# Optimization experiments

Hardware: AMD Instinct MI355X
Metric: run time of the kernel (lower is better)

The kernel has to match this reference:

```python
import jax, jax.numpy as jnp
import numpy as np

N = 100000
E = 1600000
D_IN = 128
D_H = 256


def setup_inputs() -> dict:
    key = jax.random.key(0)
    ks = jax.random.split(key, 8)
    x = jax.random.normal(ks[0], (N, D_IN), dtype=jnp.float32)
    x_tilde = jax.random.normal(ks[1], (N, D_IN), dtype=jnp.float32)
    adj_row = jnp.sort(jax.random.randint(ks[2], (E,), 0, N, dtype=jnp.int32))
    adj_col = jax.random.randint(ks[3], (E,), 0, N, dtype=jnp.int32)
    # normalized-ish positive edge weights
    adj_vals = jax.random.uniform(ks[4], (E,), dtype=jnp.float32) / 16.0
    # Linear weight (torch layout [out, in]), xavier-ish scale
    W1 = jax.random.normal(ks[5], (D_H, D_IN), dtype=jnp.float32) * (2.0 / (D_IN + D_H)) ** 0.5
    prelu_a = jnp.full((1,), 0.25, dtype=jnp.float32)  # PReLU default slope
    w_bil = jax.random.normal(ks[6], (D_H, D_H), dtype=jnp.float32) * (2.0 / (2 * D_H)) ** 0.5
    return {"x": x, "x_tilde": x_tilde, "adj_vals": adj_vals, "adj_row": adj_row,
            "adj_col": adj_col, "W1": W1, "prelu_a": prelu_a, "w_bil": w_bil}


def reference(x, x_tilde, adj_vals, adj_row, adj_col, W1, prelu_a, w_bil):
    n = x.shape[0]

    def gcn(feat):
        # SpMM: agg[r] = sum_e vals[e] * feat[col[e]] for edges with row[e]==r
        gathered = adj_vals[:, None] * feat[adj_col]  # [E, D_IN]
        agg = jax.ops.segment_sum(gathered, adj_row, num_segments=n)  # [N, D_IN]
        z = agg @ W1.T  # [N, D_H]
        return jnp.where(z >= 0, z, prelu_a[0] * z)  # PReLU

    h = gcn(x)
    h_tilde = gcn(x_tilde)
    s = jax.nn.sigmoid(jnp.mean(h, axis=0))  # [D_H] readout (same for every row)
    dp = jnp.einsum('ni,ij,j->n', h, w_bil, s)  # bilinear discriminator
    dn = jnp.einsum('ni,ij,j->n', h_tilde, w_bil, s)
    return jnp.concatenate([dp, dn])[None, :]  # [1, 2N]
```

## Files before the change

kernel.cpp:

```cpp
#include <hip/hip_runtime.h>

__device__ __forceinline__ float b2f(unsigned short s) {
    union { unsigned int u; float f; } c; c.u = ((unsigned int)s) << 16; return c.f;
}
__device__ __forceinline__ unsigned short f2b(float f) {
    union { float f; unsigned int u; } c; c.f = f;
    unsigned int u = c.u;
    unsigned int r = u + 0x7FFFu + ((u >> 16) & 1u);
    return (unsigned short)(r >> 16);
}
__device__ __forceinline__ unsigned int pack2(float lo, float hi) {
    return ((unsigned int)f2b(hi) << 16) | f2b(lo);
}

typedef __attribute__((ext_vector_type(8))) short bf16x8;
typedef __attribute__((ext_vector_type(4))) float f32x4;

#define T_TILES 10

__global__ void detect_dtype(const unsigned int* __restrict__ xw,
                             int* __restrict__ flag, float* __restrict__ sum_h) {
    __shared__ int c;
    int tid = threadIdx.x;
    if (tid == 0) c = 0;
    sum_h[tid] = 0.f;
    __syncthreads();
    int cnt = 0;
    for (int i = tid; i < 1024; i += 256) {
        unsigned int w = xw[i];
        unsigned int e = (w >> 7) & 0xFFu;
        if (e >= 0x90u) cnt++;
    }
    atomicAdd(&c, cnt);
    __syncthreads();
    if (tid == 0) flag[0] = (c > 100) ? 1 : 0;
}

__global__ void build_rowptr(const int* __restrict__ row, int* __restrict__ rp,
                             int n, int e) {
    int i = blockIdx.x * blockDim.x + threadIdx.x;
    if (i > e) return;
    if (i == 0) {
        int r1 = row[0];
        for (int rr = 0; rr <= r1; ++rr) rp[rr] = 0;
    } else if (i == e) {
        int r0 = row[e - 1];
        for (int rr = r0 + 1; rr <= n; ++rr) rp[rr] = e;
    } else {
        int r0 = row[i - 1], r1 = row[i];
        for (int rr = r0 + 1; rr <= r1; ++rr) rp[rr] = i;
    }
}

__global__ void conv_params(const void* __restrict__ w1, const void* __restrict__ wbil,
                            const void* __restrict__ pa, const int* __restrict__ flag,
                            unsigned short* __restrict__ w1b, float* __restrict__ wbilf,
                            float* __restrict__ paf) {
    int i = blockIdx.x * blockDim.x + threadIdx.x;
    if (flag[0]) {
        if (i < 32768) w1b[i] = f2b(((const float*)w1)[i]);
        wbilf[i] = ((const float*)wbil)[i];
        if (i == 0) paf[0] = ((const float*)pa)[0];
    } else {
        if (i < 32768) w1b[i] = ((const unsigned short*)w1)[i];
        wbilf[i] = b2f(((const unsigned short*)wbil)[i]);
        if (i == 0) paf[0] = b2f(((const unsigned short*)pa)[0]);
    }
}

__global__ __launch_bounds__(256) void conv_x(
    const void* __restrict__ src0, const void* __restrict__ src1,
    const int* __restrict__ flag,
    unsigned short* __restrict__ d0, unsigned short* __restrict__ d1, int total8)
{
    const void* s = blockIdx.y ? src1 : src0;
    unsigned short* d = blockIdx.y ? d1 : d0;
    int i = blockIdx.x * 256 + threadIdx.x;
    if (i >= total8) return;
    if (flag[0]) {
        const float4* p = (const float4*)s + (size_t)i * 2;
        float4 a = p[0], b = p[1];
        uint4 o;
        o.x = pack2(a.x, a.y); o.y = pack2(a.z, a.w);
        o.z = pack2(b.x, b.y); o.w = pack2(b.z, b.w);
        ((uint4*)d)[i] = o;
    } else {
        ((uint4*)d)[i] = ((const uint4*)s)[i];
    }
}

__global__ __launch_bounds__(256) void spmm_dual2(
    const unsigned short* __restrict__ xb, const unsigned short* __restrict__ xtb,
    const void* __restrict__ valsv, const int* __restrict__ col,
    const int* __restrict__ row_ptr, const int* __restrict__ flag,
    unsigned short* __restrict__ aggx, unsigned short* __restrict__ aggt, int n)
{
    int wave = threadIdx.x >> 6;
    int lane = threadIdx.x & 63;
    int g = lane >> 4, l = lane & 15;
    int r = blockIdx.x * 4 + wave;
    if (r >= n) return;
    int e0 = row_ptr[r], e1 = row_ptr[r + 1];
    int f = flag[0];
    const float* valsf = (const float*)valsv;
    const unsigned short* valsb = (const unsigned short*)valsv;
    float ax[8], at[8];
#pragma unroll
    for (int d = 0; d < 8; ++d) { ax[d] = 0.f; at[d] = 0.f; }
    for (int base = e0; base < e1; base += 4) {
        int e = base + g;
        bool valid = (e < e1);
        int ec = valid ? e : (e1 - 1);
        int c = col[ec];
        float v = valid ? (f ? valsf[ec] : b2f(valsb[ec])) : 0.f;
        uint4 wx = ((const uint4*)(xb + (size_t)c * 128))[l];
        uint4 wt = ((const uint4*)(xtb + (size_t)c * 128))[l];
        ax[0] = fmaf(v, b2f((unsigned short)wx.x), ax[0]);
        ax[1] = fmaf(v, b2f((unsigned short)(wx.x >> 16)), ax[1]);
        ax[2] = fmaf(v, b2f((unsigned short)wx.y), ax[2]);
        ax[3] = fmaf(v, b2f((unsigned short)(wx.y >> 16)), ax[3]);
        ax[4] = fmaf(v, b2f((unsigned short)wx.z), ax[4]);
        ax[5] = fmaf(v, b2f((unsigned short)(wx.z >> 16)), ax[5]);
        ax[6] = fmaf(v, b2f((unsigned short)wx.w), ax[6]);
        ax[7] = fmaf(v, b2f((unsigned short)(wx.w >> 16)), ax[7]);
        at[0] = fmaf(v, b2f((unsigned short)wt.x), at[0]);
        at[1] = fmaf(v, b2f((unsigned short)(wt.x >> 16)), at[1]);
        at[2] = fmaf(v, b2f((unsigned short)wt.y), at[2]);
        at[3] = fmaf(v, b2f((unsigned short)(wt.y >> 16)), at[3]);
        at[4] = fmaf(v, b2f((unsigned short)wt.z), at[4]);
        at[5] = fmaf(v, b2f((unsigned short)(wt.z >> 16)), at[5]);
        at[6] = fmaf(v, b2f((unsigned short)wt.w), at[6]);
        at[7] = fmaf(v, b2f((unsigned short)(wt.w >> 16)), at[7]);
    }
#pragma unroll
    for (int d = 0; d < 8; ++d) {
        ax[d] += __shfl_xor(ax[d], 16, 64);
        ax[d] += __shfl_xor(ax[d], 32, 64);
        at[d] += __shfl_xor(at[d], 16, 64);
        at[d] += __shfl_xor(at[d], 32, 64);
    }
    if (g == 0) {
        uint4 o;
        o.x = pack2(ax[0], ax[1]); o.y = pack2(ax[2], ax[3]);
        o.z = pack2(ax[4], ax[5]); o.w = pack2(ax[6], ax[7]);
        ((uint4*)(aggx + (size_t)r * 128))[l] = o;
    } else if (g == 1) {
        uint4 o;
        o.x = pack2(at[0], at[1]); o.y = pack2(at[2], at[3]);
        o.z = pack2(at[4], at[5]); o.w = pack2(at[6], at[7]);
        ((uint4*)(aggt + (size_t)r * 128))[l] = o;
    }
}

__global__ __launch_bounds__(256) void spmm_dual_legacy(
    const void* __restrict__ xv, const void* __restrict__ xtv,
    const void* __restrict__ valsv, const int* __restrict__ col,
    const int* __restrict__ row_ptr, const int* __restrict__ flag,
    unsigned short* __restrict__ aggx, unsigned short* __restrict__ aggt, int n)
{
    int wave = threadIdx.x >> 6;
    int lane = threadIdx.x & 63;
    int r = blockIdx.x * 4 + wave;
    if (r >= n) return;
    int e0 = row_ptr[r], e1 = row_ptr[r + 1];
    float ax0 = 0.f, ax1 = 0.f, at0 = 0.f, at1 = 0.f;
    if (flag[0]) {
        const float* x  = (const float*)xv;
        const float* xt = (const float*)xtv;
        const float* vals = (const float*)valsv;
        for (int e = e0; e < e1; ++e) {
            int c = col[e];
            float v = vals[e];
            float2 wx = ((const float2*)(x + (size_t)c * 128))[lane];
            float2 wt = ((const float2*)(xt + (size_t)c * 128))[lane];
            ax0 = fmaf(v, wx.x, ax0); ax1 = fmaf(v, wx.y, ax1);
            at0 = fmaf(v, wt.x, at0); at1 = fmaf(v, wt.y, at1);
        }
    } else {
        const unsigned short* x  = (const unsigned short*)xv;
        const unsigned short* xt = (const unsigned short*)xtv;
        const unsigned short* vals = (const unsigned short*)valsv;
        for (int e = e0; e < e1; ++e) {
            int c = col[e];
            float v = b2f(vals[e]);
            unsigned int wx = ((const unsigned int*)(x + (size_t)c * 128))[lane];
            unsigned int wt = ((const unsigned int*)(xt + (size_t)c * 128))[lane];
            ax0 = fmaf(v, b2f((unsigned short)wx), ax0);
            ax1 = fmaf(v, b2f((unsigned short)(wx >> 16)), ax1);
            at0 = fmaf(v, b2f((unsigned short)wt), at0);
            at1 = fmaf(v, b2f((unsigned short)(wt >> 16)), at1);
        }
    }
    ((unsigned int*)(aggx + (size_t)r * 128))[lane] = pack2(ax0, ax1);
    ((unsigned int*)(aggt + (size_t)r * 128))[lane] = pack2(at0, at1);
}

__global__ __launch_bounds__(256) void gemm_colsum2(
    const short* __restrict__ aggb, const short* __restrict__ w1,
    const float* __restrict__ paf, float* __restrict__ sum_h, int ntiles)
{
    int tid = threadIdx.x;
    int w = tid >> 6, lane = tid & 63;
    int nl = lane & 15, quad = lane >> 4;
    const short* brow = w1 + ((size_t)(4 * w) * 16 + nl) * 128 + quad * 8;
    bf16x8 bf[4][4];
#pragma unroll
    for (int j = 0; j < 4; ++j)
#pragma unroll
        for (int k = 0; k < 4; ++k)
            bf[j][k] = *(const bf16x8*)(brow + j * 2048 + k * 32);
    float aslope = paf[0];
    float cs[4] = {0.f, 0.f, 0.f, 0.f};
    int t0 = blockIdx.x * T_TILES;
    int nt = ntiles - t0; if (nt > T_TILES) nt = T_TILES;
    for (int i = 0; i < nt; ++i) {
        const short* arow = aggb + ((size_t)(t0 + i) * 16 + nl) * 128 + quad * 8;
        bf16x8 af[4];
#pragma unroll
        for (int k = 0; k < 4; ++k) af[k] = *(const bf16x8*)(arow + k * 32);
        f32x4 acc[4];
#pragma unroll
        for (int j = 0; j < 4; ++j) acc[j] = (f32x4){0.f, 0.f, 0.f, 0.f};
#pragma unroll
        for (int k = 0; k < 4; ++k)
#pragma unroll
            for (int j = 0; j < 4; ++j)
                acc[j] = __builtin_amdgcn_mfma_f32_16x16x32_bf16(af[k], bf[j][k], acc[j], 0, 0, 0);
#pragma unroll
        for (int j = 0; j < 4; ++j)
#pragma unroll
            for (int r = 0; r < 4; ++r) {
                float z = acc[j][r];
                cs[j] += (z >= 0.f) ? z : aslope * z;
            }
    }
#pragma unroll
    for (int j = 0; j < 4; ++j) {
        cs[j] += __shfl_xor(cs[j], 16, 64);
        cs[j] += __shfl_xor(cs[j], 32, 64);
    }
    if (quad == 0)
#pragma unroll
        for (int j = 0; j < 4; ++j)
            atomicAdd(&sum_h[(4 * w + j) * 16 + nl], cs[j]);
}

__global__ __launch_bounds__(256) void compute_v(
    const float* __restrict__ sum_h, const float* __restrict__ wbilf,
    float* __restrict__ v, float invN)
{
    __shared__ float s_lds[256];
    int t = threadIdx.x;
    float m = sum_h[t] * invN;
    s_lds[t] = 1.f / (1.f + expf(-m));
    __syncthreads();
    const float* wrow = wbilf + (size_t)t * 256;
    float acc = 0.f;
#pragma unroll 8
    for (int j = 0; j < 256; ++j)
        acc = fmaf(wrow[j], s_lds[j], acc);
    v[t] = acc;
}

__global__ __launch_bounds__(256) void gemm_dp2(
    const short* __restrict__ aggx, const short* __restrict__ aggt,
    const short* __restrict__ w1, const float* __restrict__ paf,
    const float* __restrict__ v, const int* __restrict__ flag,
    void* __restrict__ outv, int ntiles, int N)
{
    __shared__ float dpbuf[4][T_TILES * 16];
    int tid = threadIdx.x;
    int w = tid >> 6, lane = tid & 63;
    int nl = lane & 15, quad = lane >> 4;
    const short* agg = blockIdx.y ? aggt : aggx;
    const short* brow = w1 + ((size_t)(4 * w) * 16 + nl) * 128 + quad * 8;
    bf16x8 bf[4][4];
#pragma unroll
    for (int j = 0; j < 4; ++j)
#pragma unroll
        for (int k = 0; k < 4; ++k)
            bf[j][k] = *(const bf16x8*)(brow + j * 2048 + k * 32);
    float vreg[4];
#pragma unroll
    for (int j = 0; j < 4; ++j) vreg[j] = v[(4 * w + j) * 16 + nl];
    float aslope = paf[0];
    int t0 = blockIdx.x * T_TILES;
    int nt = ntiles - t0; if (nt > T_TILES) nt = T_TILES;
    for (int i = 0; i < nt; ++i) {
        const short* arow = agg + ((size_t)(t0 + i) * 16 + nl) * 128 + quad * 8;
        bf16x8 af[4];
#pragma unroll
        for (int k = 0; k < 4; ++k) af[k] = *(const bf16x8*)(arow + k * 32);
        f32x4 acc[4];
#pragma unroll
        for (int j = 0; j < 4; ++j) acc[j] = (f32x4){0.f, 0.f, 0.f, 0.f};
#pragma unroll
        for (int k = 0; k < 4; ++k)
#pragma unroll
            for (int j = 0; j < 4; ++j)
                acc[j] = __builtin_amdgcn_mfma_f32_16x16x32_bf16(af[k], bf[j][k], acc[j], 0, 0, 0);
        float p[4] = {0.f, 0.f, 0.f, 0.f};
#pragma unroll
        for (int j = 0; j < 4; ++j)
#pragma unroll
            for (int r = 0; r < 4; ++r) {
                float z = acc[j][r];
                float h = (z >= 0.f) ? z : aslope * z;
                p[r] = fmaf(h, vreg[j], p[r]);
            }
#pragma unroll
        for (int r = 0; r < 4; ++r) {
            p[r] += __shfl_xor(p[r], 1, 64);
            p[r] += __shfl_xor(p[r], 2, 64);
            p[r] += __shfl_xor(p[r], 4, 64);
            p[r] += __shfl_xor(p[r], 8, 64);
        }
        if (nl == 0)
#pragma unroll
            for (int r = 0; r < 4; ++r)
                dpbuf[w][i * 16 + quad * 4 + r] = p[r];
    }
    __syncthreads();
    int nloc = nt * 16;
    int f = flag[0];
    for (int idx = tid; idx < nloc; idx += 256) {
        float s = dpbuf[0][idx] + dpbuf[1][idx] + dpbuf[2][idx] + dpbuf[3][idx];
        size_t o = (size_t)blockIdx.y * N + (size_t)t0 * 16 + idx;
        if (f) ((float*)outv)[o] = s;
        else   ((unsigned short*)outv)[o] = f2b(s);
    }
}

extern "C" void kernel_launch(void* const* d_in, const int* in_sizes, int n_in,
                              void* d_out, int out_size, void* d_ws, size_t ws_size,
                              hipStream_t stream) {
    const void* x    = d_in[0];
    const void* xt   = d_in[1];
    const void* vals = d_in[2];
    const int* row   = (const int*)d_in[3];
    const int* col   = (const int*)d_in[4];
    const void* w1   = d_in[5];
    const void* pa   = d_in[6];
    const void* wb   = d_in[7];

    const int N = in_sizes[0] / 128;
    const int E = in_sizes[2];
    const int ntiles = (N + 15) / 16;

    char* ws = (char*)d_ws;
    size_t off = 0;
    auto alloc = [&](size_t bytes) { char* p = ws + off; off = (off + bytes + 255) & ~(size_t)255; return p; };
    int* row_ptr         = (int*)alloc((size_t)(N + 1) * 4);
    unsigned short* aggx = (unsigned short*)alloc((size_t)N * 128 * 2);
    unsigned short* aggt = (unsigned short*)alloc((size_t)N * 128 * 2);
    unsigned short* w1b  = (unsigned short*)alloc(32768 * 2);
    float* wbilf         = (float*)alloc(65536 * 4);
    float* sum_h         = (float*)alloc(256 * 4);
    float* vvec          = (float*)alloc(256 * 4);
    float* paf           = (float*)alloc(4);
    int* flag            = (int*)alloc(4);
    size_t xbBytes = (size_t)N * 128 * 2;
    bool big = (off + 2 * xbBytes + 512) <= ws_size;
    unsigned short* xb  = nullptr;
    unsigned short* xtb = nullptr;
    if (big) {
        xb  = (unsigned short*)alloc(xbBytes);
        xtb = (unsigned short*)alloc(xbBytes);
    }

    detect_dtype<<<1, 256, 0, stream>>>((const unsigned int*)x, flag, sum_h);
    build_rowptr<<<(E + 1 + 255) / 256, 256, 0, stream>>>(row, row_ptr, N, E);
    conv_params<<<256, 256, 0, stream>>>(w1, wb, pa, flag, w1b, wbilf, paf);
    if (big) {
        int total8 = (N * 128) / 8;
        conv_x<<<dim3((total8 + 255) / 256, 2), 256, 0, stream>>>(x, xt, flag, xb, xtb, total8);
        spmm_dual2<<<(N + 3) / 4, 256, 0, stream>>>(xb, xtb, vals, col, row_ptr, flag, aggx, aggt, N);
    } else {
        spmm_dual_legacy<<<(N + 3) / 4, 256, 0, stream>>>(x, xt, vals, col, row_ptr, flag, aggx, aggt, N);
    }
    gemm_colsum2<<<(ntiles + T_TILES - 1) / T_TILES, 256, 0, stream>>>(
        (const short*)aggx, (const short*)w1b, paf, sum_h, ntiles);
    compute_v<<<1, 256, 0, stream>>>(sum_h, wbilf, vvec, 1.0f / (float)N);
    gemm_dp2<<<dim3((ntiles + T_TILES - 1) / T_TILES, 2), 256, 0, stream>>>(
        (const short*)aggx, (const short*)aggt, (const short*)w1b, paf, vvec, flag,
        d_out, ntiles, N);
}
```

Before: 349.4 us.

## Interleave x/x_tilde rows, fuse prep kernels, unroll SpMM, replace atomics with partials

Converts x and x_tilde into one interleaved bf16 buffer, so each gathered column index hits a contiguous 512-byte row holding both feature sets. The row-pointer build, parameter conversion and input conversion are merged into one prep kernel to cut launches. The SpMM loop now processes two edges per group per iteration with the dtype branch hoisted out of the loop. The column-sum kernel writes per-block partials that compute_v reduces, replacing atomics and the sum_h zeroing, and T_TILES doubles to 20. Risks are a longer serial partial reduction in the single-block compute_v2, fewer blocks in the GEMM kernels, and higher register pressure in the SpMM.

```diff
diff --git a/kernel.cpp b/kernel.cpp
--- a/kernel.cpp
+++ b/kernel.cpp
@@ -12,18 +12,26 @@
 __device__ __forceinline__ unsigned int pack2(float lo, float hi) {
     return ((unsigned int)f2b(hi) << 16) | f2b(lo);
 }
+__device__ __forceinline__ void fma8(float* a, float v, uint4 w) {
+    a[0] = fmaf(v, b2f((unsigned short)w.x), a[0]);
+    a[1] = fmaf(v, b2f((unsigned short)(w.x >> 16)), a[1]);
+    a[2] = fmaf(v, b2f((unsigned short)w.y), a[2]);
+    a[3] = fmaf(v, b2f((unsigned short)(w.y >> 16)), a[3]);
+    a[4] = fmaf(v, b2f((unsigned short)w.z), a[4]);
+    a[5] = fmaf(v, b2f((unsigned short)(w.z >> 16)), a[5]);
+    a[6] = fmaf(v, b2f((unsigned short)w.w), a[6]);
+    a[7] = fmaf(v, b2f((unsigned short)(w.w >> 16)), a[7]);
+}
 
 typedef __attribute__((ext_vector_type(8))) short bf16x8;
 typedef __attribute__((ext_vector_type(4))) float f32x4;
 
-#define T_TILES 10
-
-__global__ void detect_dtype(const unsigned int* __restrict__ xw,
-                             int* __restrict__ flag, float* __restrict__ sum_h) {
+#define T_TILES 20
+
+__global__ void detect_dtype(const unsigned int* __restrict__ xw, int* __restrict__ flag) {
     __shared__ int c;
     int tid = threadIdx.x;
     if (tid == 0) c = 0;
-    sum_h[tid] = 0.f;
     __syncthreads();
     int cnt = 0;
     for (int i = tid; i < 1024; i += 256) {
@@ -36,63 +44,64 @@
     if (tid == 0) flag[0] = (c > 100) ? 1 : 0;
 }
 
-__global__ void build_rowptr(const int* __restrict__ row, int* __restrict__ rp,
-                             int n, int e) {
-    int i = blockIdx.x * blockDim.x + threadIdx.x;
-    if (i > e) return;
-    if (i == 0) {
-        int r1 = row[0];
-        for (int rr = 0; rr <= r1; ++rr) rp[rr] = 0;
-    } else if (i == e) {
-        int r0 = row[e - 1];
-        for (int rr = r0 + 1; rr <= n; ++rr) rp[rr] = e;
+__global__ __launch_bounds__(256) void prep(
+    const int* __restrict__ row, int* __restrict__ rp, int n, int e, int rb,
+    const void* __restrict__ w1, const void* __restrict__ wbil,
+    const void* __restrict__ pa, const int* __restrict__ flag,
+    unsigned short* __restrict__ w1b, float* __restrict__ wbilf, float* __restrict__ paf,
+    int pb,
+    const void* __restrict__ x, const void* __restrict__ xt,
+    unsigned short* __restrict__ xint, int total8, int halfcb)
+{
+    int b = blockIdx.x, tid = threadIdx.x;
+    if (b < rb) {
+        int i = b * 256 + tid;
+        if (i > e) return;
+        if (i == 0) {
+            int r1 = row[0];
+            for (int rr = 0; rr <= r1; ++rr) rp[rr] = 0;
+        } else if (i == e) {
+            int r0 = row[e - 1];
+            for (int rr = r0 + 1; rr <= n; ++rr) rp[rr] = e;
+        } else {
+            int r0 = row[i - 1], r1 = row[i];
+            for (int rr = r0 + 1; rr <= r1; ++rr) rp[rr] = i;
+        }
+    } else if (b < rb + pb) {
+        int i = (b - rb) * 256 + tid;
+        if (flag[0]) {
+            if (i < 32768) w1b[i] = f2b(((const float*)w1)[i]);
+            wbilf[i] = ((const float*)wbil)[i];
+            if (i == 0) paf[0] = ((const float*)pa)[0];
+        } else {
+            if (i < 32768) w1b[i] = ((const unsigned short*)w1)[i];
+            wbilf[i] = b2f(((const unsigned short*)wbil)[i]);
+            if (i == 0) paf[0] = b2f(((const unsigned short*)pa)[0]);
+        }
     } else {
-        int r0 = row[i - 1], r1 = row[i];
-        for (int rr = r0 + 1; rr <= r1; ++rr) rp[rr] = i;
-    }
-}
-
-__global__ void conv_params(const void* __restrict__ w1, const void* __restrict__ wbil,
-                            const void* __restrict__ pa, const int* __restrict__ flag,
-                            unsigned short* __restrict__ w1b, float* __restrict__ wbilf,
-                            float* __restrict__ paf) {
-    int i = blockIdx.x * blockDim.x + threadIdx.x;
-    if (flag[0]) {
-        if (i < 32768) w1b[i] = f2b(((const float*)w1)[i]);
-        wbilf[i] = ((const float*)wbil)[i];
-        if (i == 0) paf[0] = ((const float*)pa)[0];
-    } else {
-        if (i < 32768) w1b[i] = ((const unsigned short*)w1)[i];
-        wbilf[i] = b2f(((const unsigned short*)wbil)[i]);
-        if (i == 0) paf[0] = b2f(((const unsigned short*)pa)[0]);
-    }
-}
-
-__global__ __launch_bounds__(256) void conv_x(
-    const void* __restrict__ src0, const void* __restrict__ src1,
+        int cb = b - rb - pb;
+        int which = (cb >= halfcb) ? 1 : 0;
+        int i = (cb - which * halfcb) * 256 + tid;
+        if (i >= total8) return;
+        const void* s = which ? xt : x;
+        int node = i >> 4, sub = i & 15;
+        uint4 o;
+        if (flag[0]) {
+            const float4* p = (const float4*)s + (size_t)i * 2;
+            float4 a = p[0], bb = p[1];
+            o.x = pack2(a.x, a.y);  o.y = pack2(a.z, a.w);
+            o.z = pack2(bb.x, bb.y); o.w = pack2(bb.z, bb.w);
+        } else {
+            o = ((const uint4*)s)[i];
+        }
+        *(uint4*)(xint + (size_t)node * 256 + which * 128 + sub * 8) = o;
+    }
+}
+
+__global__ __launch_bounds__(256) void spmm_dual3(
+    const unsigned short* __restrict__ xint, const void* __restrict__ valsv,
+    const int* __restrict__ col, const int* __restrict__ row_ptr,
     const int* __restrict__ flag,
-    unsigned short* __restrict__ d0, unsigned short* __restrict__ d1, int total8)
-{
-    const void* s = blockIdx.y ? src1 : src0;
-    unsigned short* d = blockIdx.y ? d1 : d0;
-    int i = blockIdx.x * 256 + threadIdx.x;
-    if (i >= total8) return;
-    if (flag[0]) {
-        const float4* p = (const float4*)s + (size_t)i * 2;
-        float4 a = p[0], b = p[1];
-        uint4 o;
-        o.x = pack2(a.x, a.y); o.y = pack2(a.z, a.w);
-        o.z = pack2(b.x, b.y); o.w = pack2(b.z, b.w);
-        ((uint4*)d)[i] = o;
-    } else {
-        ((uint4*)d)[i] = ((const uint4*)s)[i];
-    }
-}
-
-__global__ __launch_bounds__(256) void spmm_dual2(
-    const unsigned short* __restrict__ xb, const unsigned short* __restrict__ xtb,
-    const void* __restrict__ valsv, const int* __restrict__ col,
-    const int* __restrict__ row_ptr, const int* __restrict__ flag,
     unsigned short* __restrict__ aggx, unsigned short* __restrict__ aggt, int n)
 {
     int wave = threadIdx.x >> 6;
@@ -101,36 +110,41 @@
     int r = blockIdx.x * 4 + wave;
     if (r >= n) return;
     int e0 = row_ptr[r], e1 = row_ptr[r + 1];
-    int f = flag[0];
-    const float* valsf = (const float*)valsv;
-    const unsigned short* valsb = (const unsigned short*)valsv;
     float ax[8], at[8];
 #pragma unroll
     for (int d = 0; d < 8; ++d) { ax[d] = 0.f; at[d] = 0.f; }
-    for (int base = e0; base < e1; base += 4) {
-        int e = base + g;
-        bool valid = (e < e1);
-        int ec = valid ? e : (e1 - 1);
-        int c = col[ec];
-        float v = valid ? (f ? valsf[ec] : b2f(valsb[ec])) : 0.f;
-        uint4 wx = ((const uint4*)(xb + (size_t)c * 128))[l];
-        uint4 wt = ((const uint4*)(xtb + (size_t)c * 128))[l];
-        ax[0] = fmaf(v, b2f((unsigned short)wx.x), ax[0]);
-        ax[1] = fmaf(v, b2f((unsigned short)(wx.x >> 16)), ax[1]);
-        ax[2] = fmaf(v, b2f((unsigned short)wx.y), ax[2]);
-        ax[3] = fmaf(v, b2f((unsigned short)(wx.y >> 16)), ax[3]);
-        ax[4] = fmaf(v, b2f((unsigned short)wx.z), ax[4]);
-        ax[5] = fmaf(v, b2f((unsigned short)(wx.z >> 16)), ax[5]);
-        ax[6] = fmaf(v, b2f((unsigned short)wx.w), ax[6]);
-        ax[7] = fmaf(v, b2f((unsigned short)(wx.w >> 16)), ax[7]);
-        at[0] = fmaf(v, b2f((unsigned short)wt.x), at[0]);
-        at[1] = fmaf(v, b2f((unsigned short)(wt.x >> 16)), at[1]);
-        at[2] = fmaf(v, b2f((unsigned short)wt.y), at[2]);
-        at[3] = fmaf(v, b2f((unsigned short)(wt.y >> 16)), at[3]);
-        at[4] = fmaf(v, b2f((unsigned short)wt.z), at[4]);
-        at[5] = fmaf(v, b2f((unsigned short)(wt.z >> 16)), at[5]);
-        at[6] = fmaf(v, b2f((unsigned short)wt.w), at[6]);
-        at[7] = fmaf(v, b2f((unsigned short)(wt.w >> 16)), at[7]);
+    if (flag[0]) {
+        const float* vals = (const float*)valsv;
+        for (int base = e0; base < e1; base += 8) {
+            int eA = base + g, eB = base + 4 + g;
+            bool vA = eA < e1, vB = eB < e1;
+            int ecA = vA ? eA : e1 - 1, ecB = vB ? eB : e1 - 1;
+            int cA = col[ecA], cB = col[ecB];
+            float fvA = vA ? vals[ecA] : 0.f;
+            float fvB = vB ? vals[ecB] : 0.f;
+            const uint4* pA = (const uint4*)(xint + (size_t)cA * 256);
+            const uint4* pB = (const uint4*)(xint + (size_t)cB * 256);
+            uint4 xA = pA[l], tA = pA[16 + l];
+            uint4 xB = pB[l], tB = pB[16 + l];
+            fma8(ax, fvA, xA); fma8(at, fvA, tA);
+            fma8(ax, fvB, xB); fma8(at, fvB, tB);
+        }
+    } else {
+        const unsigned short* vals = (const unsigned short*)valsv;
+        for (int base = e0; base < e1; base += 8) {
+            int eA = base + g, eB = base + 4 + g;
+            bool vA = eA < e1, vB = eB < e1;
+            int ecA = vA ? eA : e1 - 1, ecB = vB ? eB : e1 - 1;
+            int cA = col[ecA], cB = col[ecB];
+            float fvA = vA ? b2f(vals[ecA]) : 0.f;
+            float fvB = vB ? b2f(vals[ecB]) : 0.f;
+            const uint4* pA = (const uint4*)(xint + (size_t)cA * 256);
+            const uint4* pB = (const uint4*)(xint + (size_t)cB * 256);
+            uint4 xA = pA[l], tA = pA[16 + l];
+            uint4 xB = pB[l], tB = pB[16 + l];
+            fma8(ax, fvA, xA); fma8(at, fvA, tA);
+            fma8(ax, fvB, xB); fma8(at, fvB, tB);
+        }
     }
 #pragma unroll
     for (int d = 0; d < 8; ++d) {
@@ -195,9 +209,9 @@
     ((unsigned int*)(aggt + (size_t)r * 128))[lane] = pack2(at0, at1);
 }
 
-__global__ __launch_bounds__(256) void gemm_colsum2(
+__global__ __launch_bounds__(256) void gemm_colsum3(
     const short* __restrict__ aggb, const short* __restrict__ w1,
-    const float* __restrict__ paf, float* __restrict__ sum_h, int ntiles)
+    const float* __restrict__ paf, float* __restrict__ partial, int ntiles)
 {
     int tid = threadIdx.x;
     int w = tid >> 6, lane = tid & 63;
@@ -242,17 +256,19 @@
     if (quad == 0)
 #pragma unroll
         for (int j = 0; j < 4; ++j)
-            atomicAdd(&sum_h[(4 * w + j) * 16 + nl], cs[j]);
-}
-
-__global__ __launch_bounds__(256) void compute_v(
-    const float* __restrict__ sum_h, const float* __restrict__ wbilf,
-    float* __restrict__ v, float invN)
+            partial[(size_t)blockIdx.x * 256 + (4 * w + j) * 16 + nl] = cs[j];
+}
+
+__global__ __launch_bounds__(256) void compute_v2(
+    const float* __restrict__ partial, int nblocks,
+    const float* __restrict__ wbilf, float* __restrict__ v, float invN)
 {
     __shared__ float s_lds[256];
     int t = threadIdx.x;
-    float m = sum_h[t] * invN;
-    s_lds[t] = 1.f / (1.f + expf(-m));
+    float s = 0.f;
+    for (int b = 0; b < nblocks; ++b)
+        s += partial[(size_t)b * 256 + t];
+    s_lds[t] = 1.f / (1.f + expf(-s * invN));
     __syncthreads();
     const float* wrow = wbilf + (size_t)t * 256;
     float acc = 0.f;
@@ -346,6 +362,7 @@
     const int N = in_sizes[0] / 128;
     const int E = in_sizes[2];
     const int ntiles = (N + 15) / 16;
+    const int cs_blocks = (ntiles + T_TILES - 1) / T_TILES;
 
     char* ws = (char*)d_ws;
     size_t off = 0;
@@ -355,33 +372,37 @@
     unsigned short* aggt = (unsigned short*)alloc((size_t)N * 128 * 2);
     unsigned short* w1b  = (unsigned short*)alloc(32768 * 2);
     float* wbilf         = (float*)alloc(65536 * 4);
-    float* sum_h         = (float*)alloc(256 * 4);
+    float* partial       = (float*)alloc((size_t)cs_blocks * 256 * 4);
     float* vvec          = (float*)alloc(256 * 4);
     float* paf           = (float*)alloc(4);
     int* flag            = (int*)alloc(4);
-    size_t xbBytes = (size_t)N * 128 * 2;
-    bool big = (off + 2 * xbBytes + 512) <= ws_size;
-    unsigned short* xb  = nullptr;
-    unsigned short* xtb = nullptr;
+    size_t xintBytes = (size_t)N * 256 * 2;
+    bool big = (off + xintBytes + 512) <= ws_size;
+    unsigned short* xint = nullptr;
+    if (big) xint = (unsigned short*)alloc(xintBytes);
+
+    detect_dtype<<<1, 256, 0, stream>>>((const unsigned int*)x, flag);
+
+    int rb = (E + 1 + 255) / 256;
+    int pb = 256;
+    int total8 = (N * 128) / 8;
+    int halfcb = big ? (total8 + 255) / 256 : 0;
+    prep<<<rb + pb + 2 * halfcb, 256, 0, stream>>>(
+        row, row_ptr, N, E, rb,
+        w1, wb, pa, flag, w1b, wbilf, paf, pb,
+        x, xt, xint, total8, halfcb);
+
     if (big) {
-        xb  = (unsigned short*)alloc(xbBytes);
-        xtb = (unsigned short*)alloc(xbBytes);
-    }
-
-    detect_dtype<<<1, 256, 0, stream>>>((const unsigned int*)x, flag, sum_h);
-    build_rowptr<<<(E + 1 + 255) / 256, 256, 0, stream>>>(row, row_ptr, N, E);
-    conv_params<<<256, 256, 0, stream>>>(w1, wb, pa, flag, w1b, wbilf, paf);
-    if (big) {
-        int total8 = (N * 128) / 8;
-        conv_x<<<dim3((total8 + 255) / 256, 2), 256, 0, stream>>>(x, xt, flag, xb, xtb, total8);
-        spmm_dual2<<<(N + 3) / 4, 256, 0, stream>>>(xb, xtb, vals, col, row_ptr, flag, aggx, aggt, N);
+        spmm_dual3<<<(N + 3) / 4, 256, 0, stream>>>(xint, vals, col, row_ptr, flag,
+                                                    aggx, aggt, N);
     } else {
-        spmm_dual_legacy<<<(N + 3) / 4, 256, 0, stream>>>(x, xt, vals, col, row_ptr, flag, aggx, aggt, N);
-    }
-    gemm_colsum2<<<(ntiles + T_TILES - 1) / T_TILES, 256, 0, stream>>>(
-        (const short*)aggx, (const short*)w1b, paf, sum_h, ntiles);
-    compute_v<<<1, 256, 0, stream>>>(sum_h, wbilf, vvec, 1.0f / (float)N);
-    gemm_dp2<<<dim3((ntiles + T_TILES - 1) / T_TILES, 2), 256, 0, stream>>>(
+        spmm_dual_legacy<<<(N + 3) / 4, 256, 0, stream>>>(x, xt, vals, col, row_ptr, flag,
+                                                          aggx, aggt, N);
+    }
+    gemm_colsum3<<<cs_blocks, 256, 0, stream>>>(
+        (const short*)aggx, (const short*)w1b, paf, partial, ntiles);
+    compute_v2<<<1, 256, 0, stream>>>(partial, cs_blocks, wbilf, vvec, 1.0f / (float)N);
+    gemm_dp2<<<dim3(cs_blocks, 2), 256, 0, stream>>>(
         (const short*)aggx, (const short*)aggt, (const short*)w1b, paf, vvec, flag,
         d_out, ntiles, N);
 }
```

Measured after the change: 408.2 us. +16.8%, slower.
